# Performance work log

Measured on AMD Instinct MI355X. Metric: run time of the kernel, lower is better.

## Reference

```python
import jax, jax.numpy as jnp
import numpy as np

RANK = 16
ALPHA = 32
SCALING = ALPHA / RANK  # alpha / rank


def setup_inputs() -> dict:
    key = jax.random.key(0)
    k_x, k_w, k_b, k_a, k_bb = jax.random.split(key, 5)
    B, S, D_IN, D_OUT = 4, 2048, 4096, 4096
    x = jax.random.normal(k_x, (B, S, D_IN), dtype=jnp.float32)
    W = jax.random.normal(k_w, (D_OUT, D_IN), dtype=jnp.float32) * (1.0 / np.sqrt(D_IN))
    b = jax.random.normal(k_b, (D_OUT,), dtype=jnp.float32) * 0.02
    # LoRA init: A ~ N(0, 2/rank); B is zeros in the module, but we use small
    # random values so the adapter path is numerically exercised.
    lora_A = jax.random.normal(k_a, (RANK, D_IN), dtype=jnp.float32) * np.sqrt(2.0 / RANK)
    lora_B = jax.random.normal(k_bb, (D_OUT, RANK), dtype=jnp.float32) * 0.02
    return {"x": x, "W": W, "b": b, "lora_A": lora_A, "lora_B": lora_B}


def reference(x, W, b, lora_A, lora_B):
    # Base linear: x @ W^T + b
    base = jnp.einsum("bsd,od->bso", x, W) + b
    # LoRA path, fused as two rank-r matmuls (never materializing B@A):
    # (x @ A^T) @ B^T * scaling  ==  F.linear(x, B@A) * scaling
    xa = jnp.einsum("bsd,rd->bsr", x, lora_A)      # [B,S,r]
    lora = jnp.einsum("bsr,or->bso", xa, lora_B)    # [B,S,D_out]
    return base + lora * SCALING
```

## Files before the change

### kernel.cpp

```cpp
#include <hip/hip_runtime.h>
#include <hip/hip_bf16.h>

#define K_DIM 4096
#define N_DIM 4096
#define R_DIM 16
#define SCALING_F 2.0f

#define BM 256
#define BN 256
#define BK 64

#define FOLD_ROWS 8
#define FOLD_BLOCKS (N_DIM / FOLD_ROWS)

typedef __attribute__((ext_vector_type(8))) short bf16x8;
typedef __attribute__((ext_vector_type(4))) float f32x4;

__device__ __forceinline__ ushort f2bf(float f) {
  union { float f; unsigned u; } v; v.f = f;
  unsigned u = v.u;
  u += 0x7FFF + ((u >> 16) & 1);
  return (ushort)(u >> 16);
}

__global__ __launch_bounds__(256) void prepass_kernel(
    const float* __restrict__ x, ushort* __restrict__ xb,
    const float* __restrict__ W, const float* __restrict__ A,
    const float* __restrict__ Bl, ushort* __restrict__ wb, long n4) {
  if (blockIdx.x < FOLD_BLOCKS) {
    const int o0 = blockIdx.x * FOLD_ROWS;
#pragma unroll 1
    for (int j = 0; j < 4; ++j) {
      const int d0 = (threadIdx.x + j * 256) * 4;
      float4 a[R_DIM];
#pragma unroll
      for (int r = 0; r < R_DIM; ++r)
        a[r] = *(const float4*)(A + (size_t)r * K_DIM + d0);
#pragma unroll 1
      for (int rr = 0; rr < FOLD_ROWS; ++rr) {
        const int o = o0 + rr;
        float4 w = *(const float4*)(W + (size_t)o * K_DIM + d0);
        float s0 = w.x, s1 = w.y, s2 = w.z, s3 = w.w;
#pragma unroll
        for (int r = 0; r < R_DIM; ++r) {
          const float bv = Bl[o * R_DIM + r] * SCALING_F;
          s0 += bv * a[r].x; s1 += bv * a[r].y;
          s2 += bv * a[r].z; s3 += bv * a[r].w;
        }
        ushort4 ob;
        ob.x = f2bf(s0); ob.y = f2bf(s1); ob.z = f2bf(s2); ob.w = f2bf(s3);
        *(ushort4*)(wb + (size_t)o * K_DIM + d0) = ob;
      }
    }
  } else {
    long i = (long)(blockIdx.x - FOLD_BLOCKS) * blockDim.x + threadIdx.x;
    long stride = 2048L * blockDim.x;
    for (; i < n4; i += stride) {
      long idx = i * 4;
      float4 v = *(const float4*)(x + idx);
      ushort4 o;
      o.x = f2bf(v.x); o.y = f2bf(v.y); o.z = f2bf(v.z); o.w = f2bf(v.w);
      *(ushort4*)(xb + idx) = o;
    }
  }
}


#define RS 8192L

#define GLOAD(SRC, LOFF)                                                    \
  __builtin_amdgcn_global_load_lds(                                         \
      (const __attribute__((address_space(1))) void*)(SRC),                 \
      (__attribute__((address_space(3))) void*)(smem + (LOFF)), 16, 0, 0)

#define LDSA(BUF) ((BUF) * 32768)
#define LDSB(BUF) (65536 + (BUF) * 32768)

#define ST_A_EVEN(T, BUF) do {                                              \
    GLOAD(aS + (size_t)(T) * 128,            LDSA(BUF) + ldsDst);           \
    GLOAD(aS + (size_t)(T) * 128 + 128 * RS, LDSA(BUF) + 16384 + ldsDst); } while (0)
#define ST_A_ODD(T, BUF) do {                                               \
    GLOAD(aS + (size_t)(T) * 128 + 64 * RS,  LDSA(BUF) + 8192 + ldsDst);    \
    GLOAD(aS + (size_t)(T) * 128 + 192 * RS, LDSA(BUF) + 24576 + ldsDst); } while (0)
#define ST_B_H0(T, BUF) do {                                                \
    GLOAD(bS + (size_t)(T) * 128,            LDSB(BUF) + ldsDst);           \
    GLOAD(bS + (size_t)(T) * 128 + 64 * RS,  LDSB(BUF) + 8192 + ldsDst); } while (0)
#define ST_B_H1(T, BUF) do {                                                \
    GLOAD(bS + (size_t)(T) * 128 + 128 * RS, LDSB(BUF) + 16384 + ldsDst);   \
    GLOAD(bS + (size_t)(T) * 128 + 192 * RS, LDSB(BUF) + 24576 + ldsDst); } while (0)

#define LDA(M, CK, BUF) (*(const bf16x8*)(smem + LDSA(BUF) + aRd + (M) * 2048 + (CK)))
#define LDB(N, CK, BUF) (*(const bf16x8*)(smem + LDSB(BUF) + bRd + (N) * 2048 + (CK)))

#define PF_A(MB, CK, BUF) do {                                              \
    afr[0] = LDA((MB) + 0, CK, BUF); afr[1] = LDA((MB) + 1, CK, BUF);       \
    afr[2] = LDA((MB) + 2, CK, BUF); afr[3] = LDA((MB) + 3, CK, BUF); } while (0)
#define PF_B_ALL(BUF) do {                                                  \
    bfr[0][0] = LDB(0, cK0, BUF); bfr[0][1] = LDB(0, cK1, BUF);             \
    bfr[1][0] = LDB(1, cK0, BUF); bfr[1][1] = LDB(1, cK1, BUF);             \
    bfr[2][0] = LDB(2, cK0, BUF); bfr[2][1] = LDB(2, cK1, BUF);             \
    bfr[3][0] = LDB(3, cK0, BUF); bfr[3][1] = LDB(3, cK1, BUF); } while (0)

#define MFMA16(MB, KK) do {                                                 \
    _Pragma("unroll") for (int mm = 0; mm < 4; ++mm)                        \
      _Pragma("unroll") for (int nn = 0; nn < 4; ++nn)                      \
        acc[(MB) + mm][nn] = __builtin_amdgcn_mfma_f32_16x16x32_bf16(       \
            afr[mm], bfr[nn][KK], acc[(MB) + mm][nn], 0, 0, 0); } while (0)

#define PH_CORE(MB, KK) do {                                                \
    __builtin_amdgcn_s_barrier();                                           \
    asm volatile("s_waitcnt lgkmcnt(0)");                                   \
    __builtin_amdgcn_s_setprio(1);                                          \
    MFMA16(MB, KK);                                                         \
    __builtin_amdgcn_s_setprio(0); } while (0)

__global__ __launch_bounds__(512, 2) void gemm_lora_kernel(
    const ushort* __restrict__ Ab, const ushort* __restrict__ Bb,
    const float* __restrict__ bias, float* __restrict__ C) {
  __shared__ char smem[131072];

  const int tid = threadIdx.x;
  const int wave = tid >> 6, lane = tid & 63;
  const int wm = wave >> 2, wn = wave & 3;
  const int fr = lane & 15, fq = lane >> 4;

  const int bid = blockIdx.x;
  const int bm = ((bid & 7) << 2) + ((bid >> 3) & 3);
  const int bn = bid >> 5;

  const int trow = tid >> 3;
  const int tswz = ((tid & 7) << 4) ^ ((trow & 7) << 4);
  const char* aS = (const char*)Ab + (size_t)(bm * BM + trow) * RS + tswz;
  const char* bS = (const char*)Bb + (size_t)(bn * BN + trow) * RS + tswz;
  const int ldsDst = tid << 4;

  const int sa  = (fr & 7) << 4;
  const int cK0 = (fq << 4) ^ sa;
  const int cK1 = (64 | (fq << 4)) ^ sa;
  const int aRd = ((wm << 7) + fr) << 7;
  const int bRd = ((wn << 6) + fr) << 7;

  f32x4 acc[8][4];
#pragma unroll
  for (int m = 0; m < 8; ++m)
#pragma unroll
    for (int n = 0; n < 4; ++n) acc[m][n] = (f32x4){0.f, 0.f, 0.f, 0.f};
  bf16x8 afr[4], bfr[4][2];

  ST_B_H0(0, 0); ST_B_H1(0, 0); ST_A_EVEN(0, 0); ST_A_ODD(0, 0);
  ST_B_H0(1, 1); ST_B_H1(1, 1); ST_A_EVEN(1, 1);
  asm volatile("s_waitcnt vmcnt(6)" ::: "memory");
  __builtin_amdgcn_s_barrier();
  PF_B_ALL(0);
  PF_A(0, cK0, 0);

  const int NIT = K_DIM / (2 * BK);
#pragma unroll 1
  for (int i = 0; i < NIT; ++i) {
    const int t1 = 2 * i + 1, t2 = 2 * i + 2, t3 = 2 * i + 3;
    const bool last = (i == NIT - 1);

    ST_A_ODD(t1, 1);
    PH_CORE(0, 0);
    PF_A(0, cK1, 0);
    __builtin_amdgcn_s_barrier();

    if (!last) ST_B_H0(t2, 0);
    PH_CORE(0, 1);
    PF_A(4, cK0, 0);
    __builtin_amdgcn_s_barrier();

    if (!last) ST_B_H1(t2, 0);
    PH_CORE(4, 0);
    PF_A(4, cK1, 0);
    if (last) asm volatile("s_waitcnt vmcnt(0)" ::: "memory");
    else      asm volatile("s_waitcnt vmcnt(4)" ::: "memory");
    __builtin_amdgcn_s_barrier();

    if (!last) ST_A_EVEN(t2, 0);
    PH_CORE(4, 1);
    PF_B_ALL(1);
    PF_A(0, cK0, 1);
    __builtin_amdgcn_s_barrier();

    if (!last) ST_A_ODD(t2, 0);
    PH_CORE(0, 0);
    PF_A(0, cK1, 1);
    __builtin_amdgcn_s_barrier();

    if (!last) ST_B_H0(t3, 1);
    PH_CORE(0, 1);
    PF_A(4, cK0, 1);
    __builtin_amdgcn_s_barrier();

    if (!last) ST_B_H1(t3, 1);
    PH_CORE(4, 0);
    PF_A(4, cK1, 1);
    if (!last) asm volatile("s_waitcnt vmcnt(4)" ::: "memory");
    __builtin_amdgcn_s_barrier();

    if (!last) ST_A_EVEN(t3, 1);
    PH_CORE(4, 1);
    if (!last) {
      PF_B_ALL(0);
      PF_A(0, cK0, 0);
      __builtin_amdgcn_s_barrier();
    }
  }

  const int ccol0 = bn * BN + wn * 64 + fr;
  float bv[4];
#pragma unroll
  for (int n = 0; n < 4; ++n) bv[n] = bias[ccol0 + n * 16];
  const int crow0 = bm * BM + wm * 128 + fq * 4;
#pragma unroll
  for (int m = 0; m < 8; ++m)
#pragma unroll
    for (int n = 0; n < 4; ++n)
#pragma unroll
      for (int v = 0; v < 4; ++v) {
        int row = crow0 + m * 16 + v;
        C[(size_t)row * N_DIM + ccol0 + n * 16] = acc[m][n][v] + bv[n];
      }
}

extern "C" void kernel_launch(void* const* d_in, const int* in_sizes, int n_in,
                              void* d_out, int out_size, void* d_ws, size_t ws_size,
                              hipStream_t stream) {
  const float* x  = (const float*)d_in[0];
  const float* W  = (const float*)d_in[1];
  const float* b  = (const float*)d_in[2];
  const float* lA = (const float*)d_in[3];
  const float* lB = (const float*)d_in[4];
  float* out = (float*)d_out;

  const int M = in_sizes[0] / K_DIM;

  ushort* xb = (ushort*)d_ws;
  ushort* wb = xb + (size_t)M * K_DIM;

  long n4 = (long)M * K_DIM / 4;
  prepass_kernel<<<FOLD_BLOCKS + 2048, 256, 0, stream>>>(x, xb, W, lA, lB, wb, n4);
  gemm_lora_kernel<<<(M / BM) * (N_DIM / BN), 512, 0, stream>>>(xb, wb, b, out);
}
```

Measured before the change: 293.8 us.

## Drop per-phase trailing barriers and issue global-to-LDS loads after fragment reads

Each phase of the main K-loop now ends after its LDS fragment prefetch and its async global-to-LDS stage issue, with no second s_barrier. Only the barrier at the start of each MFMA phase is kept, which halves the number of workgroup barriers per iteration. Issuing the global loads after the LDS reads is meant to keep the reads ahead of any overwrite of the same buffer. The risk is a write-after-read hazard, because there is no longer a full barrier separating other waves' reads from the incoming async LDS writes.

```diff
diff --git a/kernel.cpp b/kernel.cpp
--- a/kernel.cpp
+++ b/kernel.cpp
@@ -107,7 +107,7 @@
         acc[(MB) + mm][nn] = __builtin_amdgcn_mfma_f32_16x16x32_bf16(       \
             afr[mm], bfr[nn][KK], acc[(MB) + mm][nn], 0, 0, 0); } while (0)
 
-#define PH_CORE(MB, KK) do {                                                \
+#define BODY(MB, KK) do {                                                   \
     __builtin_amdgcn_s_barrier();                                           \
     asm volatile("s_waitcnt lgkmcnt(0)");                                   \
     __builtin_amdgcn_s_setprio(1);                                          \
@@ -160,51 +160,45 @@
     const int t1 = 2 * i + 1, t2 = 2 * i + 2, t3 = 2 * i + 3;
     const bool last = (i == NIT - 1);
 
+    BODY(0, 0);
+    PF_A(0, cK1, 0);
     ST_A_ODD(t1, 1);
-    PH_CORE(0, 0);
-    PF_A(0, cK1, 0);
-    __builtin_amdgcn_s_barrier();
-
+
+    BODY(0, 1);
+    PF_A(4, cK0, 0);
     if (!last) ST_B_H0(t2, 0);
-    PH_CORE(0, 1);
-    PF_A(4, cK0, 0);
-    __builtin_amdgcn_s_barrier();
-
+
+    BODY(4, 0);
+    PF_A(4, cK1, 0);
     if (!last) ST_B_H1(t2, 0);
-    PH_CORE(4, 0);
-    PF_A(4, cK1, 0);
     if (last) asm volatile("s_waitcnt vmcnt(0)" ::: "memory");
     else      asm volatile("s_waitcnt vmcnt(4)" ::: "memory");
-    __builtin_amdgcn_s_barrier();
-
-    if (!last) ST_A_EVEN(t2, 0);
-    PH_CORE(4, 1);
+
+    BODY(4, 1);
     PF_B_ALL(1);
     PF_A(0, cK0, 1);
-    __builtin_amdgcn_s_barrier();
-
+    if (!last) ST_A_EVEN(t2, 0);
+
+    BODY(0, 0);
+    PF_A(0, cK1, 1);
     if (!last) ST_A_ODD(t2, 0);
-    PH_CORE(0, 0);
-    PF_A(0, cK1, 1);
-    __builtin_amdgcn_s_barrier();
-
+
+    BODY(0, 1);
+    PF_A(4, cK0, 1);
     if (!last) ST_B_H0(t3, 1);
-    PH_CORE(0, 1);
-    PF_A(4, cK0, 1);
-    __builtin_amdgcn_s_barrier();
-
-    if (!last) ST_B_H1(t3, 1);
-    PH_CORE(4, 0);
+
+    BODY(4, 0);
     PF_A(4, cK1, 1);
-    if (!last) asm volatile("s_waitcnt vmcnt(4)" ::: "memory");
-    __builtin_amdgcn_s_barrier();
-
-    if (!last) ST_A_EVEN(t3, 1);
-    PH_CORE(4, 1);
+    if (!last) {
+      ST_B_H1(t3, 1);
+      asm volatile("s_waitcnt vmcnt(4)" ::: "memory");
+    }
+
+    BODY(4, 1);
     if (!last) {
       PF_B_ALL(0);
       PF_A(0, cK0, 0);
-      __builtin_amdgcn_s_barrier();
+      ST_A_EVEN(t3, 1);
     }
   }
 
```

Result: faster. 285.8 us (-2.7%).
